# Kernel tuning notes

Hardware: AMD Instinct MI355X
Metric: run time of the kernel (lower is better)

Reference implementation:

```python
import jax, jax.numpy as jnp
import numpy as np

H = 64  # hidden_size
B, T1, T2, T3 = 4096, 512, 256, 128


def setup_inputs() -> dict:
    key = jax.random.key(0)
    ks = jax.random.split(key, 18)
    s = 1.0 / np.sqrt(H)  # torch LSTMCell init scale
    def p(k, shape, scale):
        return jax.random.normal(k, shape, dtype=jnp.float32) * scale
    return {
        "x1": p(ks[0], (B, T1), 1.0),
        "x2": p(ks[1], (B, T2), 1.0),
        "x3": p(ks[2], (B, T3), 1.0),
        "W_ih3": p(ks[3], (4 * H, 3), s), "W_hh3": p(ks[4], (4 * H, H), s),
        "b_ih3": p(ks[5], (4 * H,), s), "b_hh3": p(ks[6], (4 * H,), s),
        "W_ih2": p(ks[7], (4 * H, 2), s), "W_hh2": p(ks[8], (4 * H, H), s),
        "b_ih2": p(ks[9], (4 * H,), s), "b_hh2": p(ks[10], (4 * H,), s),
        "W_ih1": p(ks[11], (4 * H, 1), s), "W_hh1": p(ks[12], (4 * H, H), s),
        "b_ih1": p(ks[13], (4 * H,), s), "b_hh1": p(ks[14], (4 * H,), s),
        "W_out": p(ks[15], (1, H), s), "b_out": p(ks[16], (1,), s),
    }


def reference(x1, x2, x3,
              W_ih3, W_hh3, b_ih3, b_hh3,
              W_ih2, W_hh2, b_ih2, b_hh2,
              W_ih1, W_hh1, b_ih1, b_hh1,
              W_out, b_out):
    h = W_hh3.shape[1]
    Bb, t1 = x1.shape
    r2, r3 = t1 // x2.shape[1], t1 // x3.shape[1]
    # Pad input weights to width 3; concat order is [x1, x2, x3] (zeros where absent),
    # so padded-column zeros reproduce the narrower cells exactly.
    Wi = jnp.stack([W_ih3,
                    jnp.pad(W_ih2, ((0, 0), (0, 1))),
                    jnp.pad(W_ih1, ((0, 0), (0, 2)))])  # [3, 4H, 3]
    Wh = jnp.stack([W_hh3, W_hh2, W_hh1])               # [3, 4H, H]
    bs = jnp.stack([b_ih3 + b_hh3, b_ih2 + b_hh2, b_ih1 + b_hh1])  # [3, 4H]
    t = np.arange(t1)
    has2 = (t % r2 == 0)
    has3 = (t % r3 == 0)
    assert not np.any(has3 & ~has2), "ratio2 must divide ratio3 for the concat-order mapping"
    # width 3 -> cell3 (type 0), width 2 -> cell2 (type 1), width 1 -> cell1 (type 2)
    step_type = jnp.asarray(2 - has2.astype(np.int32) - has3.astype(np.int32))
    xs = jnp.zeros((t1, Bb, 3), x1.dtype)
    xs = xs.at[:, :, 0].set(x1.T)
    xs = xs.at[::r2, :, 1].set(x2.T)
    xs = xs.at[::r3, :, 2].set(x3.T)

    def step(carry, inp):
        hx, cx = carry
        x, ty = inp
        g = x @ Wi[ty].T + hx @ Wh[ty].T + bs[ty]  # [B, 4H]
        i, f, gg, o = jnp.split(g, 4, axis=-1)     # torch gate order i,f,g,o
        cx = jax.nn.sigmoid(f) * cx + jax.nn.sigmoid(i) * jnp.tanh(gg)
        hx = jax.nn.sigmoid(o) * jnp.tanh(cx)
        return (hx, cx), None

    z = jnp.zeros((Bb, h), x1.dtype)
    (hx, _), _ = jax.lax.scan(step, (z, z), (xs, step_type))
    return jax.nn.sigmoid(hx @ W_out.T + b_out)  # [B, 1]
```

## Files before the change

### kernel.cpp

```cpp
#include <hip/hip_runtime.h>


typedef __attribute__((ext_vector_type(8))) short short8v;
typedef __attribute__((ext_vector_type(4))) float float4v;

template <int N> struct IC { static constexpr int value = N; };

#define AST 72
#define XS1 516
#define XS2 260
#define XS3 132

#if __has_builtin(__builtin_amdgcn_exp2f)
#define EXP2F(x) __builtin_amdgcn_exp2f(x)
#else
#define EXP2F(x) exp2f(x)
#endif
#if __has_builtin(__builtin_amdgcn_rcpf)
#define RCPF(x) __builtin_amdgcn_rcpf(x)
#else
#define RCPF(x) (1.0f / (x))
#endif

#define NL2E -1.4426950408889634f
#define NL2E2 -2.8853900817779268f

__device__ __forceinline__ short f2bf(float f) {
  union { float f; unsigned u; } v; v.f = f;
  unsigned r = v.u + 0x7FFFu + ((v.u >> 16) & 1u);
  return (short)(r >> 16);
}
__device__ __forceinline__ float bf2f(short h) {
  union { float f; unsigned u; } v;
  v.u = ((unsigned)(unsigned short)h) << 16;
  return v.f;
}
__device__ __forceinline__ float rcp1p(float y) {
  return RCPF(1.0f + EXP2F(y));
}
__device__ __forceinline__ float fsig(float x) { return rcp1p(x * NL2E); }
__device__ __forceinline__ float ftanh(float x) {
  return __builtin_fmaf(2.0f, rcp1p(x * NL2E2), -1.0f);
}

__global__ __launch_bounds__(256, 1) void mlstm_kernel(
    const float* __restrict__ x1, const float* __restrict__ x2,
    const float* __restrict__ x3,
    const float* __restrict__ Wi3, const float* __restrict__ Wh3,
    const float* __restrict__ bi3, const float* __restrict__ bh3,
    const float* __restrict__ Wi2, const float* __restrict__ Wh2,
    const float* __restrict__ bi2, const float* __restrict__ bh2,
    const float* __restrict__ Wi1, const float* __restrict__ Wh1,
    const float* __restrict__ bi1, const float* __restrict__ bh1,
    const float* __restrict__ Wout, const float* __restrict__ bout,
    float* __restrict__ out) {
  __shared__ __attribute__((aligned(16))) short Ab0[16 * AST];
  __shared__ __attribute__((aligned(16))) short Ab1[16 * AST];
  __shared__ short x1b[16 * XS1];
  __shared__ short x2b[16 * XS2];
  __shared__ short x3b[16 * XS3];

  const int tid = threadIdx.x;
  const int w = tid >> 6;
  const int lane = tid & 63;
  const int q = lane >> 4;
  const int c = lane & 15;
  const int R0 = blockIdx.x << 4;

  for (int idx = tid; idx < 16 * 512; idx += 256) {
    int m = idx >> 9, t = idx & 511;
    x1b[m * XS1 + t] = f2bf(x1[(size_t)(R0 + m) * 512 + t]);
  }
  for (int idx = tid; idx < 16 * 256; idx += 256) {
    int m = idx >> 8, t = idx & 255;
    x2b[m * XS2 + t] = f2bf(x2[(size_t)(R0 + m) * 256 + t]);
  }
  for (int idx = tid; idx < 16 * 128; idx += 256) {
    int m = idx >> 7, t = idx & 127;
    x3b[m * XS3 + t] = f2bf(x3[(size_t)(R0 + m) * 128 + t]);
  }
  for (int idx = tid; idx < 16 * AST; idx += 256) {
    Ab0[idx] = 0;
    Ab1[idx] = 0;
  }

  short8v whs[3][4][2];
  short8v wix[3][4];
  float4v bias4[3][4];
  {
    const float* WhA[3] = {Wh3, Wh2, Wh1};
    const float* WiA[3] = {Wi3, Wi2, Wi1};
    const float* biA[3] = {bi3, bi2, bi1};
    const float* bhA[3] = {bh3, bh2, bh1};
    const int wdt[3] = {3, 2, 1};
#pragma unroll
    for (int ty = 0; ty < 3; ++ty) {
#pragma unroll
      for (int g = 0; g < 4; ++g) {
        const float sg = (g == 2) ? NL2E2 : NL2E;
        const int n = g * 64 + 16 * w + c;
#pragma unroll
        for (int kf = 0; kf < 2; ++kf) {
          short8v v;
#pragma unroll
          for (int j = 0; j < 8; ++j)
            v[j] = f2bf(sg * WhA[ty][n * 64 + kf * 32 + q * 8 + j]);
          whs[ty][g][kf] = v;
        }
        short8v v2 = {0, 0, 0, 0, 0, 0, 0, 0};
        if (q == 0) {
#pragma unroll
          for (int j = 0; j < 3; ++j)
            if (j < wdt[ty]) v2[j] = f2bf(sg * WiA[ty][n * wdt[ty] + j]);
        }
        wix[ty][g] = v2;
        float b = sg * (biA[ty][n] + bhA[ty][n]);
        float4v bv = {b, b, b, b};
        bias4[ty][g] = bv;
      }
    }
  }

  const int afo = c * AST + q * 8;
  const int hwo = (4 * q) * AST + 16 * w + c;
  const int x1o = c * XS1;
  const int x2o = c * XS2;
  const int x3o = c * XS3;

  __syncthreads();

  float cx[4] = {0.f, 0.f, 0.f, 0.f};

  auto stepf = [&](auto tyc, int t, const short* rbuf, short* wbuf) {
    constexpr int TY = decltype(tyc)::value;
    short hx1 = x1b[x1o + t];
    short hx2 = x2b[x2o + (t >> 1)];
    short hx3 = x3b[x3o + (t >> 2)];
    short8v a2 = {hx1, hx2, hx3, 0, 0, 0, 0, 0};
    short8v a0 = *(const short8v*)(rbuf + afo);
    short8v a1 = *(const short8v*)(rbuf + afo + 32);

    float4v acc[4];
#pragma unroll
    for (int g = 0; g < 4; ++g) {
      float4v z = bias4[TY][g];
      z = __builtin_amdgcn_mfma_f32_16x16x32_bf16(a0, whs[TY][g][0], z, 0, 0, 0);
      z = __builtin_amdgcn_mfma_f32_16x16x32_bf16(a1, whs[TY][g][1], z, 0, 0, 0);
      z = __builtin_amdgcn_mfma_f32_16x16x32_bf16(a2, wix[TY][g], z, 0, 0, 0);
      acc[g] = z;
    }

    short* hb = wbuf + hwo;
#pragma unroll
    for (int r = 0; r < 4; ++r) {
      float si = rcp1p(acc[0][r]);
      float sf = rcp1p(acc[1][r]);
      float tg = __builtin_fmaf(2.0f, rcp1p(acc[2][r]), -1.0f);
      float so = rcp1p(acc[3][r]);
      float ncx = __builtin_fmaf(sf, cx[r], si * tg);
      cx[r] = ncx;
      float hv = so * ftanh(ncx);
      hb[r * AST] = f2bf(hv);
    }
    __syncthreads();
  };

  for (int t4 = 0; t4 < 512; t4 += 4) {
    stepf(IC<0>{}, t4, Ab0, Ab1);
    stepf(IC<2>{}, t4 + 1, Ab1, Ab0);
    stepf(IC<1>{}, t4 + 2, Ab0, Ab1);
    stepf(IC<2>{}, t4 + 3, Ab1, Ab0);
  }

  if (tid < 16) {
    float s = bout[0];
    const short* hr = Ab0 + tid * AST;
#pragma unroll
    for (int k = 0; k < 64; ++k)
      s = __builtin_fmaf(bf2f(hr[k]), Wout[k], s);
    out[R0 + tid] = fsig(s);
  }
}

extern "C" void kernel_launch(void* const* d_in, const int* in_sizes, int n_in,
                              void* d_out, int out_size, void* d_ws,
                              size_t ws_size, hipStream_t stream) {
  const float* x1 = (const float*)d_in[0];
  const float* x2 = (const float*)d_in[1];
  const float* x3 = (const float*)d_in[2];
  const float* Wi3 = (const float*)d_in[3];
  const float* Wh3 = (const float*)d_in[4];
  const float* bi3 = (const float*)d_in[5];
  const float* bh3 = (const float*)d_in[6];
  const float* Wi2 = (const float*)d_in[7];
  const float* Wh2 = (const float*)d_in[8];
  const float* bi2 = (const float*)d_in[9];
  const float* bh2 = (const float*)d_in[10];
  const float* Wi1 = (const float*)d_in[11];
  const float* Wh1 = (const float*)d_in[12];
  const float* bi1 = (const float*)d_in[13];
  const float* bh1 = (const float*)d_in[14];
  const float* Wout = (const float*)d_in[15];
  const float* bout = (const float*)d_in[16];
  float* out = (float*)d_out;

  hipLaunchKernelGGL(mlstm_kernel, dim3(256), dim3(256), 0, stream,
                     x1, x2, x3, Wi3, Wh3, bi3, bh3, Wi2, Wh2, bi2, bh2,
                     Wi1, Wh1, bi1, bh1, Wout, bout, out);
}
```

Measured before the change: 333.2 us.

## Split LSTM gates across two wave groups with LDS exchange, 512-thread blocks

Doubles the block to 512 threads so each of 8 waves computes two of the four gates instead of all four. Gate activations go through a shared-memory exchange buffer, and each wave then updates cell state for half the rows. This shortens the per-wave MFMA and transcendental chain on the serial recurrence path. In exchange it adds a second barrier per step, extra LDS traffic, and a single h buffer instead of ping-pong. It also prefetches the next step's x inputs.

Result: slower. 376.8 us (+13.1%).

```diff
diff --git a/kernel.cpp b/kernel.cpp
--- a/kernel.cpp
+++ b/kernel.cpp
@@ -3,10 +3,13 @@
 
 typedef __attribute__((ext_vector_type(8))) short short8v;
 typedef __attribute__((ext_vector_type(4))) float float4v;
+typedef __attribute__((ext_vector_type(2))) float float2v;
 
 template <int N> struct IC { static constexpr int value = N; };
 
 #define AST 72
+#define HP 65
+#define PLANE (16 * HP)
 #define XS1 516
 #define XS2 260
 #define XS3 132
@@ -39,11 +42,8 @@
   return RCPF(1.0f + EXP2F(y));
 }
 __device__ __forceinline__ float fsig(float x) { return rcp1p(x * NL2E); }
-__device__ __forceinline__ float ftanh(float x) {
-  return __builtin_fmaf(2.0f, rcp1p(x * NL2E2), -1.0f);
-}
-
-__global__ __launch_bounds__(256, 1) void mlstm_kernel(
+
+__global__ __launch_bounds__(512, 2) void mlstm_kernel(
     const float* __restrict__ x1, const float* __restrict__ x2,
     const float* __restrict__ x3,
     const float* __restrict__ Wi3, const float* __restrict__ Wh3,
@@ -54,39 +54,38 @@
     const float* __restrict__ bi1, const float* __restrict__ bh1,
     const float* __restrict__ Wout, const float* __restrict__ bout,
     float* __restrict__ out) {
-  __shared__ __attribute__((aligned(16))) short Ab0[16 * AST];
-  __shared__ __attribute__((aligned(16))) short Ab1[16 * AST];
+  __shared__ __attribute__((aligned(16))) short Ab[16 * AST];
+  __shared__ __attribute__((aligned(16))) float2v actb[2 * PLANE];
   __shared__ short x1b[16 * XS1];
   __shared__ short x2b[16 * XS2];
   __shared__ short x3b[16 * XS3];
 
   const int tid = threadIdx.x;
-  const int w = tid >> 6;
+  const int wid = tid >> 6;
   const int lane = tid & 63;
   const int q = lane >> 4;
   const int c = lane & 15;
+  const int p = wid & 3;
+  const int u = wid >> 2;
   const int R0 = blockIdx.x << 4;
 
-  for (int idx = tid; idx < 16 * 512; idx += 256) {
+  for (int idx = tid; idx < 16 * 512; idx += 512) {
     int m = idx >> 9, t = idx & 511;
     x1b[m * XS1 + t] = f2bf(x1[(size_t)(R0 + m) * 512 + t]);
   }
-  for (int idx = tid; idx < 16 * 256; idx += 256) {
+  for (int idx = tid; idx < 16 * 256; idx += 512) {
     int m = idx >> 8, t = idx & 255;
     x2b[m * XS2 + t] = f2bf(x2[(size_t)(R0 + m) * 256 + t]);
   }
-  for (int idx = tid; idx < 16 * 128; idx += 256) {
+  for (int idx = tid; idx < 16 * 128; idx += 512) {
     int m = idx >> 7, t = idx & 127;
     x3b[m * XS3 + t] = f2bf(x3[(size_t)(R0 + m) * 128 + t]);
   }
-  for (int idx = tid; idx < 16 * AST; idx += 256) {
-    Ab0[idx] = 0;
-    Ab1[idx] = 0;
-  }
-
-  short8v whs[3][4][2];
-  short8v wix[3][4];
-  float4v bias4[3][4];
+  for (int idx = tid; idx < 16 * AST; idx += 512) Ab[idx] = 0;
+
+  short8v whs[3][2][2];
+  short8v wix[3][2];
+  float bia[3][2];
   {
     const float* WhA[3] = {Wh3, Wh2, Wh1};
     const float* WiA[3] = {Wi3, Wi2, Wi1};
@@ -96,16 +95,17 @@
 #pragma unroll
     for (int ty = 0; ty < 3; ++ty) {
 #pragma unroll
-      for (int g = 0; g < 4; ++g) {
+      for (int i = 0; i < 2; ++i) {
+        const int g = 2 * u + i;
         const float sg = (g == 2) ? NL2E2 : NL2E;
-        const int n = g * 64 + 16 * w + c;
+        const int n = g * 64 + 16 * p + c;
 #pragma unroll
         for (int kf = 0; kf < 2; ++kf) {
           short8v v;
 #pragma unroll
           for (int j = 0; j < 8; ++j)
             v[j] = f2bf(sg * WhA[ty][n * 64 + kf * 32 + q * 8 + j]);
-          whs[ty][g][kf] = v;
+          whs[ty][i][kf] = v;
         }
         short8v v2 = {0, 0, 0, 0, 0, 0, 0, 0};
         if (q == 0) {
@@ -113,68 +113,82 @@
           for (int j = 0; j < 3; ++j)
             if (j < wdt[ty]) v2[j] = f2bf(sg * WiA[ty][n * wdt[ty] + j]);
         }
-        wix[ty][g] = v2;
-        float b = sg * (biA[ty][n] + bhA[ty][n]);
-        float4v bv = {b, b, b, b};
-        bias4[ty][g] = bv;
+        wix[ty][i] = v2;
+        bia[ty][i] = sg * (biA[ty][n] + bhA[ty][n]);
       }
     }
   }
 
+  const float kA = u ? 2.0f : 1.0f;
+  const float kB = u ? -1.0f : 0.0f;
+
   const int afo = c * AST + q * 8;
-  const int hwo = (4 * q) * AST + 16 * w + c;
-  const int x1o = c * XS1;
-  const int x2o = c * XS2;
-  const int x3o = c * XS3;
+  const int awo = u * PLANE + (4 * q) * HP + 16 * p + c;
+  const int m0 = u * 8 + q, m1 = m0 + 4;
+  const int hcol = 16 * p + c;
+  const int aro0 = m0 * HP + hcol, aro1 = m1 * HP + hcol;
+  const int hwo0 = m0 * AST + hcol, hwo1 = m1 * AST + hcol;
+  const int x1o = c * XS1, x2o = c * XS2, x3o = c * XS3;
 
   __syncthreads();
 
-  float cx[4] = {0.f, 0.f, 0.f, 0.f};
-
-  auto stepf = [&](auto tyc, int t, const short* rbuf, short* wbuf) {
+  float cx0 = 0.f, cx1 = 0.f;
+  short px1 = x1b[x1o], px2 = x2b[x2o], px3 = x3b[x3o];
+
+  auto stepf = [&](auto tyc, int t) {
     constexpr int TY = decltype(tyc)::value;
-    short hx1 = x1b[x1o + t];
-    short hx2 = x2b[x2o + (t >> 1)];
-    short hx3 = x3b[x3o + (t >> 2)];
-    short8v a2 = {hx1, hx2, hx3, 0, 0, 0, 0, 0};
-    short8v a0 = *(const short8v*)(rbuf + afo);
-    short8v a1 = *(const short8v*)(rbuf + afo + 32);
-
-    float4v acc[4];
-#pragma unroll
-    for (int g = 0; g < 4; ++g) {
-      float4v z = bias4[TY][g];
-      z = __builtin_amdgcn_mfma_f32_16x16x32_bf16(a0, whs[TY][g][0], z, 0, 0, 0);
-      z = __builtin_amdgcn_mfma_f32_16x16x32_bf16(a1, whs[TY][g][1], z, 0, 0, 0);
-      z = __builtin_amdgcn_mfma_f32_16x16x32_bf16(a2, wix[TY][g], z, 0, 0, 0);
-      acc[g] = z;
-    }
-
-    short* hb = wbuf + hwo;
+    __syncthreads();
+    short8v a0 = *(const short8v*)(Ab + afo);
+    short8v a1 = *(const short8v*)(Ab + afo + 32);
+    short8v a2 = {px1, px2, px3, 0, 0, 0, 0, 0};
+    int tn = t + 1;
+    if (tn > 511) tn = 511;
+    px1 = x1b[x1o + tn];
+    px2 = x2b[x2o + (tn >> 1)];
+    px3 = x3b[x3o + (tn >> 2)];
+
+    float b0 = bia[TY][0], b1 = bia[TY][1];
+    float4v z0 = {b0, b0, b0, b0};
+    float4v z1 = {b1, b1, b1, b1};
+    z0 = __builtin_amdgcn_mfma_f32_16x16x32_bf16(a0, whs[TY][0][0], z0, 0, 0, 0);
+    z1 = __builtin_amdgcn_mfma_f32_16x16x32_bf16(a0, whs[TY][1][0], z1, 0, 0, 0);
+    z0 = __builtin_amdgcn_mfma_f32_16x16x32_bf16(a1, whs[TY][0][1], z0, 0, 0, 0);
+    z1 = __builtin_amdgcn_mfma_f32_16x16x32_bf16(a1, whs[TY][1][1], z1, 0, 0, 0);
+    z0 = __builtin_amdgcn_mfma_f32_16x16x32_bf16(a2, wix[TY][0], z0, 0, 0, 0);
+    z1 = __builtin_amdgcn_mfma_f32_16x16x32_bf16(a2, wix[TY][1], z1, 0, 0, 0);
 #pragma unroll
     for (int r = 0; r < 4; ++r) {
-      float si = rcp1p(acc[0][r]);
-      float sf = rcp1p(acc[1][r]);
-      float tg = __builtin_fmaf(2.0f, rcp1p(acc[2][r]), -1.0f);
-      float so = rcp1p(acc[3][r]);
-      float ncx = __builtin_fmaf(sf, cx[r], si * tg);
-      cx[r] = ncx;
-      float hv = so * ftanh(ncx);
-      hb[r * AST] = f2bf(hv);
+      float gA = __builtin_fmaf(kA, rcp1p(z0[r]), kB);
+      float gB = rcp1p(z1[r]);
+      float2v pr = {gA, gB};
+      actb[awo + r * HP] = pr;
     }
     __syncthreads();
+    float2v if0 = actb[aro0];
+    float2v go0 = actb[PLANE + aro0];
+    float2v if1 = actb[aro1];
+    float2v go1 = actb[PLANE + aro1];
+    float n0 = __builtin_fmaf(if0.y, cx0, if0.x * go0.x);
+    cx0 = n0;
+    float h0 = go0.y * __builtin_fmaf(2.0f, rcp1p(n0 * NL2E2), -1.0f);
+    Ab[hwo0] = f2bf(h0);
+    float n1 = __builtin_fmaf(if1.y, cx1, if1.x * go1.x);
+    cx1 = n1;
+    float h1 = go1.y * __builtin_fmaf(2.0f, rcp1p(n1 * NL2E2), -1.0f);
+    Ab[hwo1] = f2bf(h1);
   };
 
   for (int t4 = 0; t4 < 512; t4 += 4) {
-    stepf(IC<0>{}, t4, Ab0, Ab1);
-    stepf(IC<2>{}, t4 + 1, Ab1, Ab0);
-    stepf(IC<1>{}, t4 + 2, Ab0, Ab1);
-    stepf(IC<2>{}, t4 + 3, Ab1, Ab0);
-  }
+    stepf(IC<0>{}, t4);
+    stepf(IC<2>{}, t4 + 1);
+    stepf(IC<1>{}, t4 + 2);
+    stepf(IC<2>{}, t4 + 3);
+  }
+  __syncthreads();
 
   if (tid < 16) {
     float s = bout[0];
-    const short* hr = Ab0 + tid * AST;
+    const short* hr = Ab + tid * AST;
 #pragma unroll
     for (int k = 0; k < 64; ++k)
       s = __builtin_fmaf(bf2f(hr[k]), Wout[k], s);
@@ -204,7 +218,7 @@
   const float* bout = (const float*)d_in[16];
   float* out = (float*)d_out;
 
-  hipLaunchKernelGGL(mlstm_kernel, dim3(256), dim3(256), 0, stream,
+  hipLaunchKernelGGL(mlstm_kernel, dim3(256), dim3(512), 0, stream,
                      x1, x2, x3, Wi3, Wh3, bi3, bh3, Wi2, Wh2, bi2, bh2,
                      Wi1, Wh1, bi1, bh1, Wout, bout, out);
 }
```

## Double waves per block splitting gate rows, fuse sigmoid/tanh reciprocals

Applied to the files above, without the earlier changes.

Launches 512 threads per block (8 waves) in place of 4. Each pair of waves computes the same MFMA gate tiles redundantly, and each wave handles only half of the accumulator rows in the element-wise LSTM update. The gate activations are rewritten to share one reciprocal per product (sigmoid·tanh combined), with clamps added to keep exp2 finite. This cuts the serial transcendental latency per step at the cost of duplicated MFMA work and a larger barrier.

Result: slower. 393.7 us (+18.2%).

```diff
diff --git a/kernel.cpp b/kernel.cpp
--- a/kernel.cpp
+++ b/kernel.cpp
@@ -39,11 +39,11 @@
   return RCPF(1.0f + EXP2F(y));
 }
 __device__ __forceinline__ float fsig(float x) { return rcp1p(x * NL2E); }
-__device__ __forceinline__ float ftanh(float x) {
-  return __builtin_fmaf(2.0f, rcp1p(x * NL2E2), -1.0f);
-}
-
-__global__ __launch_bounds__(256, 1) void mlstm_kernel(
+__device__ __forceinline__ float clamp126(float y) {
+  return fminf(fmaxf(y, -126.f), 126.f);
+}
+
+__global__ __launch_bounds__(512, 2) void mlstm_kernel(
     const float* __restrict__ x1, const float* __restrict__ x2,
     const float* __restrict__ x3,
     const float* __restrict__ Wi3, const float* __restrict__ Wh3,
@@ -61,32 +61,34 @@
   __shared__ short x3b[16 * XS3];
 
   const int tid = threadIdx.x;
-  const int w = tid >> 6;
+  const int wid = tid >> 6;
   const int lane = tid & 63;
   const int q = lane >> 4;
   const int c = lane & 15;
+  const int p = wid & 3;
+  const int s = wid >> 2;
   const int R0 = blockIdx.x << 4;
 
-  for (int idx = tid; idx < 16 * 512; idx += 256) {
+  for (int idx = tid; idx < 16 * 512; idx += 512) {
     int m = idx >> 9, t = idx & 511;
     x1b[m * XS1 + t] = f2bf(x1[(size_t)(R0 + m) * 512 + t]);
   }
-  for (int idx = tid; idx < 16 * 256; idx += 256) {
+  for (int idx = tid; idx < 16 * 256; idx += 512) {
     int m = idx >> 8, t = idx & 255;
     x2b[m * XS2 + t] = f2bf(x2[(size_t)(R0 + m) * 256 + t]);
   }
-  for (int idx = tid; idx < 16 * 128; idx += 256) {
+  for (int idx = tid; idx < 16 * 128; idx += 512) {
     int m = idx >> 7, t = idx & 127;
     x3b[m * XS3 + t] = f2bf(x3[(size_t)(R0 + m) * 128 + t]);
   }
-  for (int idx = tid; idx < 16 * AST; idx += 256) {
+  for (int idx = tid; idx < 16 * AST; idx += 512) {
     Ab0[idx] = 0;
     Ab1[idx] = 0;
   }
 
   short8v whs[3][4][2];
   short8v wix[3][4];
-  float4v bias4[3][4];
+  float bia[3][4];
   {
     const float* WhA[3] = {Wh3, Wh2, Wh1};
     const float* WiA[3] = {Wi3, Wi2, Wi1};
@@ -98,7 +100,7 @@
 #pragma unroll
       for (int g = 0; g < 4; ++g) {
         const float sg = (g == 2) ? NL2E2 : NL2E;
-        const int n = g * 64 + 16 * w + c;
+        const int n = g * 64 + 16 * p + c;
 #pragma unroll
         for (int kf = 0; kf < 2; ++kf) {
           short8v v;
@@ -114,22 +116,18 @@
             if (j < wdt[ty]) v2[j] = f2bf(sg * WiA[ty][n * wdt[ty] + j]);
         }
         wix[ty][g] = v2;
-        float b = sg * (biA[ty][n] + bhA[ty][n]);
-        float4v bv = {b, b, b, b};
-        bias4[ty][g] = bv;
+        bia[ty][g] = sg * (biA[ty][n] + bhA[ty][n]);
       }
     }
   }
 
   const int afo = c * AST + q * 8;
-  const int hwo = (4 * q) * AST + 16 * w + c;
-  const int x1o = c * XS1;
-  const int x2o = c * XS2;
-  const int x3o = c * XS3;
+  const int hwo = (4 * q + 2 * s) * AST + 16 * p + c;
+  const int x1o = c * XS1, x2o = c * XS2, x3o = c * XS3;
 
   __syncthreads();
 
-  float cx[4] = {0.f, 0.f, 0.f, 0.f};
+  float cx[2] = {0.f, 0.f};
 
   auto stepf = [&](auto tyc, int t, const short* rbuf, short* wbuf) {
     constexpr int TY = decltype(tyc)::value;
@@ -143,7 +141,8 @@
     float4v acc[4];
 #pragma unroll
     for (int g = 0; g < 4; ++g) {
-      float4v z = bias4[TY][g];
+      float b = bia[TY][g];
+      float4v z = {b, b, b, b};
       z = __builtin_amdgcn_mfma_f32_16x16x32_bf16(a0, whs[TY][g][0], z, 0, 0, 0);
       z = __builtin_amdgcn_mfma_f32_16x16x32_bf16(a1, whs[TY][g][1], z, 0, 0, 0);
       z = __builtin_amdgcn_mfma_f32_16x16x32_bf16(a2, wix[TY][g], z, 0, 0, 0);
@@ -152,15 +151,19 @@
 
     short* hb = wbuf + hwo;
 #pragma unroll
-    for (int r = 0; r < 4; ++r) {
-      float si = rcp1p(acc[0][r]);
-      float sf = rcp1p(acc[1][r]);
-      float tg = __builtin_fmaf(2.0f, rcp1p(acc[2][r]), -1.0f);
-      float so = rcp1p(acc[3][r]);
-      float ncx = __builtin_fmaf(sf, cx[r], si * tg);
-      cx[r] = ncx;
-      float hv = so * ftanh(ncx);
-      hb[r * AST] = f2bf(hv);
+    for (int rr = 0; rr < 2; ++rr) {
+      const int ai = 2 * s + rr;
+      float Ei = EXP2F(acc[0][ai]);
+      float Ef = EXP2F(acc[1][ai]);
+      float Eg = EXP2F(clamp126(acc[2][ai]));
+      float Eo = EXP2F(acc[3][ai]);
+      float sitg = (1.0f - Eg) * RCPF((1.0f + Ei) * (1.0f + Eg));
+      float sf = RCPF(1.0f + Ef);
+      float ncx = __builtin_fmaf(sf, cx[rr], sitg);
+      cx[rr] = ncx;
+      float Ec = EXP2F(clamp126(ncx * NL2E2));
+      float hv = (1.0f - Ec) * RCPF((1.0f + Eo) * (1.0f + Ec));
+      hb[rr * AST] = f2bf(hv);
     }
     __syncthreads();
   };
@@ -173,12 +176,12 @@
   }
 
   if (tid < 16) {
-    float s = bout[0];
+    float sum = bout[0];
     const short* hr = Ab0 + tid * AST;
 #pragma unroll
     for (int k = 0; k < 64; ++k)
-      s = __builtin_fmaf(bf2f(hr[k]), Wout[k], s);
-    out[R0 + tid] = fsig(s);
+      sum = __builtin_fmaf(bf2f(hr[k]), Wout[k], sum);
+    out[R0 + tid] = fsig(sum);
   }
 }
 
@@ -204,7 +207,7 @@
   const float* bout = (const float*)d_in[16];
   float* out = (float*)d_out;
 
-  hipLaunchKernelGGL(mlstm_kernel, dim3(256), dim3(256), 0, stream,
+  hipLaunchKernelGGL(mlstm_kernel, dim3(256), dim3(512), 0, stream,
                      x1, x2, x3, Wi3, Wh3, bi3, bh3, Wi2, Wh2, bi2, bh2,
                      Wi1, Wh1, bi1, bh1, Wout, bout, out);
 }
```
